# Optimization experiments

Hardware: AMD Instinct MI355X
Metric: run time of the kernel (lower is better)

## Reference

```python
import jax, jax.numpy as jnp
import numpy as np
from jax.scipy.special import logsumexp

N_ITERS = 20


def setup_inputs() -> dict:
    key = jax.random.key(0)
    k1, _ = jax.random.split(key)
    cost_matrix = jax.random.uniform(k1, (64, 1024, 1024), dtype=jnp.float32)
    epsilon = jnp.ones((1,), dtype=jnp.float32)
    return {"cost_matrix": cost_matrix, "epsilon": epsilon}


def reference(cost_matrix, epsilon):
    # log-space Sinkhorn: alternate row / column normalization in log domain
    log_alpha = -cost_matrix / epsilon  # (B, N, N)

    def step(la, _):
        la = la - logsumexp(la, axis=-1, keepdims=True)  # row normalize
        la = la - logsumexp(la, axis=-2, keepdims=True)  # col normalize
        return la, None

    log_alpha, _ = jax.lax.scan(step, log_alpha, None, length=N_ITERS)
    return jnp.exp(log_alpha)
```

## Files before the change

kernel.cpp:

```cpp
#include <hip/hip_runtime.h>
#include <hip/hip_fp16.h>


#define BATCH 64
#define N 1024
#define NITERS 20
#define RPB 64
#define BPB 16
#define NBLK (BATCH * BPB)
#define THREADS 256
#define NU2 (N / 4)
#define NU4 (N / 8)
#define NU4F8 (N / 16)
#define NGRP 64
#define CSUM_ELEMS ((size_t)NITERS * BATCH * N)
#define BAR_WORDS 128

typedef float f32x2 __attribute__((ext_vector_type(2)));

union H2U { __half2 h; unsigned u; };

__device__ __forceinline__ float4 h4_to_f4(uint2 r) {
    H2U a, b;
    a.u = r.x; b.u = r.y;
    float2 fa = __half22float2(a.h);
    float2 fb = __half22float2(b.h);
    return make_float4(fa.x, fa.y, fb.x, fb.y);
}

__device__ __forceinline__ void h8_unpack(uint4 r, float* f) {
    H2U a, b, c, d;
    a.u = r.x; b.u = r.y; c.u = r.z; d.u = r.w;
    float2 fa = __half22float2(a.h), fb = __half22float2(b.h);
    float2 fc = __half22float2(c.h), fd = __half22float2(d.h);
    f[0] = fa.x; f[1] = fa.y; f[2] = fb.x; f[3] = fb.y;
    f[4] = fc.x; f[5] = fc.y; f[6] = fd.x; f[7] = fd.y;
}

__device__ __forceinline__ uint4 h8_pack(const float* f) {
    H2U a, b, c, d;
    a.h = __float22half2_rn(make_float2(f[0], f[1]));
    b.h = __float22half2_rn(make_float2(f[2], f[3]));
    c.h = __float22half2_rn(make_float2(f[4], f[5]));
    d.h = __float22half2_rn(make_float2(f[6], f[7]));
    uint4 r; r.x = a.u; r.y = b.u; r.z = c.u; r.w = d.u;
    return r;
}

__device__ __forceinline__ uint4 pack_fp8_16(const float* k) {
    uint4 r;
    int a;
    a = __builtin_amdgcn_cvt_pk_fp8_f32(k[0],  k[1],  0, false);
    a = __builtin_amdgcn_cvt_pk_fp8_f32(k[2],  k[3],  a, true);
    r.x = (unsigned)a;
    a = __builtin_amdgcn_cvt_pk_fp8_f32(k[4],  k[5],  0, false);
    a = __builtin_amdgcn_cvt_pk_fp8_f32(k[6],  k[7],  a, true);
    r.y = (unsigned)a;
    a = __builtin_amdgcn_cvt_pk_fp8_f32(k[8],  k[9],  0, false);
    a = __builtin_amdgcn_cvt_pk_fp8_f32(k[10], k[11], a, true);
    r.z = (unsigned)a;
    a = __builtin_amdgcn_cvt_pk_fp8_f32(k[12], k[13], 0, false);
    a = __builtin_amdgcn_cvt_pk_fp8_f32(k[14], k[15], a, true);
    r.w = (unsigned)a;
    return r;
}

__device__ __forceinline__ void unpack_fp8_16(uint4 r, float* f) {
    f32x2 p;
    p = __builtin_amdgcn_cvt_pk_f32_fp8((int)r.x, false); f[0]  = p.x; f[1]  = p.y;
    p = __builtin_amdgcn_cvt_pk_f32_fp8((int)r.x, true);  f[2]  = p.x; f[3]  = p.y;
    p = __builtin_amdgcn_cvt_pk_f32_fp8((int)r.y, false); f[4]  = p.x; f[5]  = p.y;
    p = __builtin_amdgcn_cvt_pk_f32_fp8((int)r.y, true);  f[6]  = p.x; f[7]  = p.y;
    p = __builtin_amdgcn_cvt_pk_f32_fp8((int)r.z, false); f[8]  = p.x; f[9]  = p.y;
    p = __builtin_amdgcn_cvt_pk_f32_fp8((int)r.z, true);  f[10] = p.x; f[11] = p.y;
    p = __builtin_amdgcn_cvt_pk_f32_fp8((int)r.w, false); f[12] = p.x; f[13] = p.y;
    p = __builtin_amdgcn_cvt_pk_f32_fp8((int)r.w, true);  f[14] = p.x; f[15] = p.y;
}

__global__ __launch_bounds__(THREADS) void sk_zero(float* __restrict__ csum_all,
                                                   int total) {
    const int i = blockIdx.x * THREADS + threadIdx.x;
    if (i < total) csum_all[i] = 0.0f;
}

__device__ __forceinline__ void gbar(unsigned* __restrict__ bar,
                                     unsigned& gencount) {
    __syncthreads();
    if (threadIdx.x == 0) {
        __threadfence();
        unsigned* grp    = bar;
        unsigned* master = bar + NGRP;
        unsigned* gen    = bar + NGRP + 1;
        const unsigned gid = blockIdx.x & (NGRP - 1);
        if (atomicAdd(&grp[gid], 1u) == (NBLK / NGRP) - 1u) {
            if (atomicAdd(master, 1u) == NGRP - 1u) {
                #pragma unroll
                for (int i = 0; i < NGRP; ++i) atomicExch(&grp[i], 0u);
                atomicExch(master, 0u);
                __threadfence();
                atomicAdd(gen, 1u);
            }
        }
        while (__hip_atomic_load(gen, __ATOMIC_RELAXED,
                                 __HIP_MEMORY_SCOPE_AGENT) == gencount)
            __builtin_amdgcn_s_sleep(2);
        __threadfence();
    }
    __syncthreads();
    ++gencount;
}

__global__ __launch_bounds__(THREADS, 4) void sk_fused(
        const float* __restrict__ C, const float* __restrict__ eps,
        uint4* __restrict__ K16, uint4* __restrict__ K8,
        float* __restrict__ csum, unsigned* __restrict__ bar,
        float* __restrict__ out) {
    __shared__ float4 smc[4][N / 4];
    __shared__ float u_lds[RPB];
    const int t = threadIdx.x;
    const int lane = t & 63, w = t >> 6;
    const int bid = blockIdx.x;
    const int b = bid >> 4, bx = bid & 15;
    const int row0 = bx * RPB + w * 16;
    const int tt = (t + 16 * bx) & 255;
    unsigned gencount = 0;

    {
        const float nie = -1.0f / eps[0];
        const float4* __restrict__ Cp =
            (const float4*)(C + ((size_t)b * N + row0) * N) + lane * 4;
        uint4* __restrict__ Kp16 = K16 + ((size_t)b * N + row0) * NU4 + lane * 2;
        uint4* __restrict__ Kp8  = K8  + ((size_t)b * N + row0) * NU4F8 + lane;

        float colacc[16];
        #pragma unroll
        for (int q = 0; q < 16; ++q) colacc[q] = 0.0f;

        float4 cur[4];
        #pragma unroll
        for (int q = 0; q < 4; ++q) cur[q] = Cp[q];

        #pragma unroll
        for (int i = 0; i < 16; ++i) {
            float4 nxt[4];
            if (i < 15) {
                #pragma unroll
                for (int q = 0; q < 4; ++q) nxt[q] = Cp[(i + 1) * (N / 4) + q];
            }
            float k[16];
            const float* cf = (const float*)cur;
            #pragma unroll
            for (int q = 0; q < 16; ++q) k[q] = __expf(cf[q] * nie);

            Kp16[(size_t)i * NU4]     = h8_pack(k);
            Kp16[(size_t)i * NU4 + 1] = h8_pack(k + 8);
            Kp8[(size_t)i * NU4F8]    = pack_fp8_16(k);

            float s = (((k[0] + k[1]) + (k[2] + k[3])) + ((k[4] + k[5]) + (k[6] + k[7])))
                    + (((k[8] + k[9]) + (k[10] + k[11])) + ((k[12] + k[13]) + (k[14] + k[15])));
            #pragma unroll
            for (int off = 32; off; off >>= 1) s += __shfl_xor(s, off, 64);
            const float ui = 1.0f / s;

            #pragma unroll
            for (int q = 0; q < 16; ++q) colacc[q] += k[q] * ui;

            if (i < 15) {
                #pragma unroll
                for (int q = 0; q < 4; ++q) cur[q] = nxt[q];
            }
        }

        #pragma unroll
        for (int q = 0; q < 4; ++q)
            smc[w][lane * 4 + q] = make_float4(colacc[4 * q], colacc[4 * q + 1],
                                               colacc[4 * q + 2], colacc[4 * q + 3]);
        __syncthreads();
        float4 s0 = smc[0][tt], s1 = smc[1][tt], s2 = smc[2][tt], s3 = smc[3][tt];
        float* cs = csum + b * N + 4 * tt;
        atomicAdd(cs + 0, (s0.x + s1.x) + (s2.x + s3.x));
        atomicAdd(cs + 1, (s0.y + s1.y) + (s2.y + s3.y));
        atomicAdd(cs + 2, (s0.z + s1.z) + (s2.z + s3.z));
        atomicAdd(cs + 3, (s0.w + s1.w) + (s2.w + s3.w));
    }
    gbar(bar, gencount);

    const uint4* __restrict__ Kp8r = K8 + ((size_t)b * N + row0) * NU4F8 + lane;
    #pragma unroll 1
    for (int p = 1; p <= 18; ++p) {
        const float4* __restrict__ cin =
            (const float4*)(csum + (size_t)(p - 1) * BATCH * N + b * N) + lane * 4;
        float vv[16];
        #pragma unroll
        for (int q = 0; q < 4; ++q) {
            float4 c = cin[q];
            vv[4 * q + 0] = 1.0f / c.x;
            vv[4 * q + 1] = 1.0f / c.y;
            vv[4 * q + 2] = 1.0f / c.z;
            vv[4 * q + 3] = 1.0f / c.w;
        }

        float colacc[16];
        #pragma unroll
        for (int q = 0; q < 16; ++q) colacc[q] = 0.0f;

        uint4 buf[4];
        #pragma unroll
        for (int q = 0; q < 4; ++q) buf[q] = Kp8r[(size_t)q * NU4F8];

        __syncthreads();
        #pragma unroll
        for (int i = 0; i < 16; ++i) {
            uint4 nx;
            if (i < 12) nx = Kp8r[(size_t)(i + 4) * NU4F8];

            float k[16];
            unpack_fp8_16(buf[i & 3], k);

            float pa = (k[0] * vv[0] + k[1] * vv[1]) + (k[2] * vv[2] + k[3] * vv[3]);
            float pb = (k[4] * vv[4] + k[5] * vv[5]) + (k[6] * vv[6] + k[7] * vv[7]);
            float pc = (k[8] * vv[8] + k[9] * vv[9]) + (k[10] * vv[10] + k[11] * vv[11]);
            float pd = (k[12] * vv[12] + k[13] * vv[13]) + (k[14] * vv[14] + k[15] * vv[15]);
            float s = (pa + pb) + (pc + pd);

            #pragma unroll
            for (int off = 32; off; off >>= 1) s += __shfl_xor(s, off, 64);
            const float ui = 1.0f / s;

            #pragma unroll
            for (int q = 0; q < 16; ++q) colacc[q] += k[q] * ui;

            if (i < 12) buf[i & 3] = nx;
        }

        #pragma unroll
        for (int q = 0; q < 4; ++q)
            smc[w][lane * 4 + q] = make_float4(colacc[4 * q], colacc[4 * q + 1],
                                               colacc[4 * q + 2], colacc[4 * q + 3]);
        __syncthreads();
        float4 s0 = smc[0][tt], s1 = smc[1][tt], s2 = smc[2][tt], s3 = smc[3][tt];
        float* cs = csum + (size_t)p * BATCH * N + b * N + 4 * tt;
        atomicAdd(cs + 0, (s0.x + s1.x) + (s2.x + s3.x));
        atomicAdd(cs + 1, (s0.y + s1.y) + (s2.y + s3.y));
        atomicAdd(cs + 2, (s0.z + s1.z) + (s2.z + s3.z));
        atomicAdd(cs + 3, (s0.w + s1.w) + (s2.w + s3.w));
        gbar(bar, gencount);
    }

    {
        const float4* __restrict__ cin =
            (const float4*)(csum + (size_t)18 * BATCH * N + b * N) + lane * 4;
        float vv[16];
        #pragma unroll
        for (int q = 0; q < 4; ++q) {
            float4 c = cin[q];
            vv[4 * q + 0] = 1.0f / c.x;
            vv[4 * q + 1] = 1.0f / c.y;
            vv[4 * q + 2] = 1.0f / c.z;
            vv[4 * q + 3] = 1.0f / c.w;
        }

        const uint4* __restrict__ Kp = K16 + ((size_t)b * N + row0) * NU4 + lane * 2;

        float colacc[16];
        #pragma unroll
        for (int q = 0; q < 16; ++q) colacc[q] = 0.0f;

        uint4 c0 = Kp[0], c1 = Kp[1];
        #pragma unroll
        for (int i = 0; i < 16; ++i) {
            uint4 n0, n1;
            if (i < 15) {
                n0 = Kp[(size_t)(i + 1) * NU4];
                n1 = Kp[(size_t)(i + 1) * NU4 + 1];
            }
            float k[16];
            h8_unpack(c0, k);
            h8_unpack(c1, k + 8);

            float pa = (k[0] * vv[0] + k[1] * vv[1]) + (k[2] * vv[2] + k[3] * vv[3]);
            float pb = (k[4] * vv[4] + k[5] * vv[5]) + (k[6] * vv[6] + k[7] * vv[7]);
            float pc = (k[8] * vv[8] + k[9] * vv[9]) + (k[10] * vv[10] + k[11] * vv[11]);
            float pd = (k[12] * vv[12] + k[13] * vv[13]) + (k[14] * vv[14] + k[15] * vv[15]);
            float s = (pa + pb) + (pc + pd);

            #pragma unroll
            for (int off = 32; off; off >>= 1) s += __shfl_xor(s, off, 64);
            const float ui = 1.0f / s;
            if (lane == 0) u_lds[w * 16 + i] = ui;

            #pragma unroll
            for (int q = 0; q < 16; ++q) colacc[q] += k[q] * ui;

            if (i < 15) { c0 = n0; c1 = n1; }
        }

        #pragma unroll
        for (int q = 0; q < 4; ++q)
            smc[w][lane * 4 + q] = make_float4(colacc[4 * q], colacc[4 * q + 1],
                                               colacc[4 * q + 2], colacc[4 * q + 3]);
        __syncthreads();
        float4 s0 = smc[0][tt], s1 = smc[1][tt], s2 = smc[2][tt], s3 = smc[3][tt];
        float* cs = csum + (size_t)19 * BATCH * N + b * N + 4 * tt;
        atomicAdd(cs + 0, (s0.x + s1.x) + (s2.x + s3.x));
        atomicAdd(cs + 1, (s0.y + s1.y) + (s2.y + s3.y));
        atomicAdd(cs + 2, (s0.z + s1.z) + (s2.z + s3.z));
        atomicAdd(cs + 3, (s0.w + s1.w) + (s2.w + s3.w));
    }
    gbar(bar, gencount);

    {
        const float4 ci = ((const float4*)(csum + (size_t)19 * BATCH * N + b * N))[t];
        const float4 vv = make_float4(1.0f / ci.x, 1.0f / ci.y,
                                      1.0f / ci.z, 1.0f / ci.w);
        const size_t rowbase = (size_t)b * N + (size_t)bx * RPB;
        const uint2* __restrict__ K2 = (const uint2*)K16;

        uint2 kc = K2[rowbase * NU2 + t];
        for (int r = 0; r < RPB; ++r) {
            uint2 kn;
            if (r < RPB - 1) kn = K2[(rowbase + r + 1) * NU2 + t];
            const float ur = u_lds[r];
            float4 k = h4_to_f4(kc);
            float4 o;
            o.x = k.x * ur * vv.x;
            o.y = k.y * ur * vv.y;
            o.z = k.z * ur * vv.z;
            o.w = k.w * ur * vv.w;
            ((float4*)(out + (rowbase + r) * N))[t] = o;
            kc = kn;
        }
    }
}


__global__ __launch_bounds__(THREADS) void sk_build(
        const float* __restrict__ C, const float* __restrict__ eps,
        uint4* __restrict__ K16, uint4* __restrict__ K8,
        float* __restrict__ u, float* __restrict__ csum_out) {
    __shared__ float4 smc[4][N / 4];
    const int t = threadIdx.x;
    const int lane = t & 63, w = t >> 6;
    const int b = blockIdx.y;
    const int row0 = blockIdx.x * RPB + w * 16;
    const float nie = -1.0f / eps[0];

    const float4* __restrict__ Cp =
        (const float4*)(C + ((size_t)b * N + row0) * N) + lane * 4;
    uint4* __restrict__ Kp16 = K16 + ((size_t)b * N + row0) * NU4 + lane * 2;
    uint4* __restrict__ Kp8  = K8  + ((size_t)b * N + row0) * NU4F8 + lane;

    float colacc[16];
    #pragma unroll
    for (int q = 0; q < 16; ++q) colacc[q] = 0.0f;

    float4 cur[4];
    #pragma unroll
    for (int q = 0; q < 4; ++q) cur[q] = Cp[q];

    for (int i = 0; i < 16; ++i) {
        float4 nxt[4];
        if (i < 15) {
            #pragma unroll
            for (int q = 0; q < 4; ++q) nxt[q] = Cp[(i + 1) * (N / 4) + q];
        }
        float k[16];
        const float* cf = (const float*)cur;
        #pragma unroll
        for (int q = 0; q < 16; ++q) k[q] = __expf(cf[q] * nie);

        Kp16[(size_t)i * NU4]     = h8_pack(k);
        Kp16[(size_t)i * NU4 + 1] = h8_pack(k + 8);
        Kp8[(size_t)i * NU4F8]    = pack_fp8_16(k);

        float s = (((k[0] + k[1]) + (k[2] + k[3])) + ((k[4] + k[5]) + (k[6] + k[7])))
                + (((k[8] + k[9]) + (k[10] + k[11])) + ((k[12] + k[13]) + (k[14] + k[15])));
        #pragma unroll
        for (int off = 32; off; off >>= 1) s += __shfl_xor(s, off, 64);
        const float ui = 1.0f / s;
        if (lane == 0) u[b * N + row0 + i] = ui;

        #pragma unroll
        for (int q = 0; q < 16; ++q) colacc[q] += k[q] * ui;

        if (i < 15) {
            #pragma unroll
            for (int q = 0; q < 4; ++q) cur[q] = nxt[q];
        }
    }

    #pragma unroll
    for (int q = 0; q < 4; ++q)
        smc[w][lane * 4 + q] = make_float4(colacc[4 * q], colacc[4 * q + 1],
                                           colacc[4 * q + 2], colacc[4 * q + 3]);
    __syncthreads();
    float4 s0 = smc[0][t], s1 = smc[1][t], s2 = smc[2][t], s3 = smc[3][t];
    float* cs = csum_out + b * N + 4 * t;
    atomicAdd(cs + 0, (s0.x + s1.x) + (s2.x + s3.x));
    atomicAdd(cs + 1, (s0.y + s1.y) + (s2.y + s3.y));
    atomicAdd(cs + 2, (s0.z + s1.z) + (s2.z + s3.z));
    atomicAdd(cs + 3, (s0.w + s1.w) + (s2.w + s3.w));
}

__global__ __launch_bounds__(THREADS) void sk_iter8(
        const uint4* __restrict__ K8, const float* __restrict__ csum_in,
        float* __restrict__ csum_out) {
    __shared__ float4 smc[4][N / 4];
    const int t = threadIdx.x;
    const int lane = t & 63, w = t >> 6;
    const int b = blockIdx.y;
    const int row0 = blockIdx.x * RPB + w * 16;

    const float4* __restrict__ cin = (const float4*)(csum_in + b * N) + lane * 4;
    float vv[16];
    #pragma unroll
    for (int q = 0; q < 4; ++q) {
        float4 c = cin[q];
        vv[4 * q + 0] = 1.0f / c.x;
        vv[4 * q + 1] = 1.0f / c.y;
        vv[4 * q + 2] = 1.0f / c.z;
        vv[4 * q + 3] = 1.0f / c.w;
    }

    const uint4* __restrict__ Kp = K8 + ((size_t)b * N + row0) * NU4F8 + lane;

    float colacc[16];
    #pragma unroll
    for (int q = 0; q < 16; ++q) colacc[q] = 0.0f;

    uint4 c0 = Kp[0];
    uint4 c1 = Kp[NU4F8];
    for (int i = 0; i < 16; ++i) {
        uint4 c2;
        if (i < 14) c2 = Kp[(size_t)(i + 2) * NU4F8];

        float k[16];
        unpack_fp8_16(c0, k);

        float pa = (k[0] * vv[0] + k[1] * vv[1]) + (k[2] * vv[2] + k[3] * vv[3]);
        float pb = (k[4] * vv[4] + k[5] * vv[5]) + (k[6] * vv[6] + k[7] * vv[7]);
        float pc = (k[8] * vv[8] + k[9] * vv[9]) + (k[10] * vv[10] + k[11] * vv[11]);
        float pd = (k[12] * vv[12] + k[13] * vv[13]) + (k[14] * vv[14] + k[15] * vv[15]);
        float s = (pa + pb) + (pc + pd);

        #pragma unroll
        for (int off = 32; off; off >>= 1) s += __shfl_xor(s, off, 64);
        const float ui = 1.0f / s;

        #pragma unroll
        for (int q = 0; q < 16; ++q) colacc[q] += k[q] * ui;

        c0 = c1;
        if (i < 14) c1 = c2;
    }

    #pragma unroll
    for (int q = 0; q < 4; ++q)
        smc[w][lane * 4 + q] = make_float4(colacc[4 * q], colacc[4 * q + 1],
                                           colacc[4 * q + 2], colacc[4 * q + 3]);
    __syncthreads();
    float4 s0 = smc[0][t], s1 = smc[1][t], s2 = smc[2][t], s3 = smc[3][t];
    float* cs = csum_out + b * N + 4 * t;
    atomicAdd(cs + 0, (s0.x + s1.x) + (s2.x + s3.x));
    atomicAdd(cs + 1, (s0.y + s1.y) + (s2.y + s3.y));
    atomicAdd(cs + 2, (s0.z + s1.z) + (s2.z + s3.z));
    atomicAdd(cs + 3, (s0.w + s1.w) + (s2.w + s3.w));
}

__global__ __launch_bounds__(THREADS) void sk_iter(
        const uint4* __restrict__ K, const float* __restrict__ csum_in,
        float* __restrict__ u, float* __restrict__ csum_out) {
    __shared__ float4 smc[4][N / 4];
    const int t = threadIdx.x;
    const int lane = t & 63, w = t >> 6;
    const int b = blockIdx.y;
    const int row0 = blockIdx.x * RPB + w * 16;

    const float4* __restrict__ cin = (const float4*)(csum_in + b * N) + lane * 4;
    float vv[16];
    #pragma unroll
    for (int q = 0; q < 4; ++q) {
        float4 c = cin[q];
        vv[4 * q + 0] = 1.0f / c.x;
        vv[4 * q + 1] = 1.0f / c.y;
        vv[4 * q + 2] = 1.0f / c.z;
        vv[4 * q + 3] = 1.0f / c.w;
    }

    const uint4* __restrict__ Kp = K + ((size_t)b * N + row0) * NU4 + lane * 2;

    float colacc[16];
    #pragma unroll
    for (int q = 0; q < 16; ++q) colacc[q] = 0.0f;

    uint4 c0 = Kp[0], c1 = Kp[1];
    for (int i = 0; i < 16; ++i) {
        uint4 n0, n1;
        if (i < 15) {
            n0 = Kp[(size_t)(i + 1) * NU4];
            n1 = Kp[(size_t)(i + 1) * NU4 + 1];
        }
        float k[16];
        h8_unpack(c0, k);
        h8_unpack(c1, k + 8);

        float pa = (k[0] * vv[0] + k[1] * vv[1]) + (k[2] * vv[2] + k[3] * vv[3]);
        float pb = (k[4] * vv[4] + k[5] * vv[5]) + (k[6] * vv[6] + k[7] * vv[7]);
        float pc = (k[8] * vv[8] + k[9] * vv[9]) + (k[10] * vv[10] + k[11] * vv[11]);
        float pd = (k[12] * vv[12] + k[13] * vv[13]) + (k[14] * vv[14] + k[15] * vv[15]);
        float s = (pa + pb) + (pc + pd);

        #pragma unroll
        for (int off = 32; off; off >>= 1) s += __shfl_xor(s, off, 64);
        const float ui = 1.0f / s;
        if (lane == 0) u[b * N + row0 + i] = ui;

        #pragma unroll
        for (int q = 0; q < 16; ++q) colacc[q] += k[q] * ui;

        if (i < 15) { c0 = n0; c1 = n1; }
    }

    #pragma unroll
    for (int q = 0; q < 4; ++q)
        smc[w][lane * 4 + q] = make_float4(colacc[4 * q], colacc[4 * q + 1],
                                           colacc[4 * q + 2], colacc[4 * q + 3]);
    __syncthreads();
    float4 s0 = smc[0][t], s1 = smc[1][t], s2 = smc[2][t], s3 = smc[3][t];
    float* cs = csum_out + b * N + 4 * t;
    atomicAdd(cs + 0, (s0.x + s1.x) + (s2.x + s3.x));
    atomicAdd(cs + 1, (s0.y + s1.y) + (s2.y + s3.y));
    atomicAdd(cs + 2, (s0.z + s1.z) + (s2.z + s3.z));
    atomicAdd(cs + 3, (s0.w + s1.w) + (s2.w + s3.w));
}

__global__ __launch_bounds__(THREADS) void sk_final(
        const uint2* __restrict__ K, const float* __restrict__ u,
        const float* __restrict__ csum_last, float* __restrict__ out) {
    const int t = threadIdx.x;
    const int row = blockIdx.x;
    const int b = blockIdx.y;
    const float ui = u[b * N + row];
    const float4 ci = ((const float4*)(csum_last + b * N))[t];
    const float4 vv = make_float4(1.0f / ci.x, 1.0f / ci.y, 1.0f / ci.z, 1.0f / ci.w);
    const size_t base = (size_t)b * N + row;
    float4 k = h4_to_f4((K + base * NU2)[t]);
    float4 o;
    o.x = k.x * ui * vv.x;
    o.y = k.y * ui * vv.y;
    o.z = k.z * ui * vv.z;
    o.w = k.w * ui * vv.w;
    ((float4*)(out + base * N))[t] = o;
}


__device__ __forceinline__ float block_reduce_broadcast(float val, float* lds) {
    #pragma unroll
    for (int off = 32; off > 0; off >>= 1)
        val += __shfl_xor(val, off, 64);
    const int lane = threadIdx.x & 63;
    const int wid  = threadIdx.x >> 6;
    if (lane == 0) lds[wid] = val;
    __syncthreads();
    float total = lds[0] + lds[1] + lds[2] + lds[3];
    __syncthreads();
    return total;
}

__global__ __launch_bounds__(THREADS) void sink_init(float* __restrict__ v,
                                                     float* __restrict__ colsum) {
    const int i = blockIdx.x * THREADS + threadIdx.x;
    v[i] = 1.0f;
    colsum[i] = 0.0f;
}

__global__ __launch_bounds__(THREADS) void sink_iter(
        const float* __restrict__ C, const float* __restrict__ eps,
        const float* __restrict__ v, float* __restrict__ u,
        float* __restrict__ colsum) {
    __shared__ float lds[4];
    const int t = threadIdx.x;
    const int b = blockIdx.y;
    const int row0 = blockIdx.x * RPB;
    const float neg_inv_eps = -1.0f / eps[0];

    const float4 vv = ((const float4*)(v + b * N))[t];
    const float4* __restrict__ Cp = (const float4*)(C + ((size_t)b * N + row0) * N);

    float4 colacc = make_float4(0.f, 0.f, 0.f, 0.f);
    float4 cur = Cp[t];
    for (int i = 0; i < RPB; ++i) {
        float4 nxt = cur;
        if (i + 1 < RPB)
            nxt = Cp[(size_t)(i + 1) * (N / 4) + t];

        float4 k;
        k.x = __expf(cur.x * neg_inv_eps);
        k.y = __expf(cur.y * neg_inv_eps);
        k.z = __expf(cur.z * neg_inv_eps);
        k.w = __expf(cur.w * neg_inv_eps);

        float s = k.x * vv.x + k.y * vv.y + k.z * vv.z + k.w * vv.w;
        float S = block_reduce_broadcast(s, lds);
        float ui = 1.0f / S;
        if (t == 0) u[b * N + row0 + i] = ui;

        colacc.x += k.x * ui;
        colacc.y += k.y * ui;
        colacc.z += k.z * ui;
        colacc.w += k.w * ui;
        cur = nxt;
    }

    float* cs = colsum + b * N + 4 * t;
    atomicAdd(cs + 0, colacc.x);
    atomicAdd(cs + 1, colacc.y);
    atomicAdd(cs + 2, colacc.z);
    atomicAdd(cs + 3, colacc.w);
}

__global__ __launch_bounds__(THREADS) void sink_fix(float* __restrict__ v,
                                                    float* __restrict__ colsum) {
    const int i = blockIdx.x * THREADS + threadIdx.x;
    v[i] = 1.0f / colsum[i];
    colsum[i] = 0.0f;
}

__global__ __launch_bounds__(THREADS) void sink_final(
        const float* __restrict__ C, const float* __restrict__ eps,
        const float* __restrict__ u, const float* __restrict__ v,
        float* __restrict__ out) {
    const int t = threadIdx.x;
    const int row = blockIdx.x;
    const int b = blockIdx.y;
    const float neg_inv_eps = -1.0f / eps[0];
    const float ui = u[b * N + row];
    const float4 vv = ((const float4*)(v + b * N))[t];
    const size_t base = ((size_t)b * N + row) * N;
    float4 c = ((const float4*)(C + base))[t];
    float4 o;
    o.x = __expf(c.x * neg_inv_eps) * ui * vv.x;
    o.y = __expf(c.y * neg_inv_eps) * ui * vv.y;
    o.z = __expf(c.z * neg_inv_eps) * ui * vv.z;
    o.w = __expf(c.w * neg_inv_eps) * ui * vv.w;
    ((float4*)(out + base))[t] = o;
}


extern "C" void kernel_launch(void* const* d_in, const int* in_sizes, int n_in,
                              void* d_out, int out_size, void* d_ws, size_t ws_size,
                              hipStream_t stream) {
    const float* C   = (const float*)d_in[0];
    const float* eps = (const float*)d_in[1];
    float* out = (float*)d_out;

    const size_t k16_bytes = (size_t)BATCH * N * N * 2;
    const size_t k8_bytes  = (size_t)BATCH * N * N;
    const size_t uv_elems  = (size_t)BATCH * N;
    const size_t needed    = k16_bytes + k8_bytes +
                             (CSUM_ELEMS + BAR_WORDS + uv_elems) * 4;

    if (ws_size >= needed) {
        uint4* K16 = (uint4*)d_ws;
        uint4* K8  = (uint4*)((char*)d_ws + k16_bytes);
        float* csum = (float*)((char*)d_ws + k16_bytes + k8_bytes);
        unsigned* bar = (unsigned*)(csum + CSUM_ELEMS);
        float* u = (float*)(bar + BAR_WORDS);

        static int coop_ok = -1;
        if (coop_ok < 0) {
            int nb = 0;
            hipError_t e = hipOccupancyMaxActiveBlocksPerMultiprocessor(
                &nb, sk_fused, THREADS, 0);
            coop_ok = (e == hipSuccess && nb >= 4) ? 1 : 0;
        }

        const int zero_total = (int)(CSUM_ELEMS + BAR_WORDS);
        sk_zero<<<dim3((zero_total + THREADS - 1) / THREADS), dim3(THREADS),
                  0, stream>>>(csum, zero_total);

        if (coop_ok) {
            sk_fused<<<dim3(NBLK), dim3(THREADS), 0, stream>>>(
                C, eps, K16, K8, csum, bar, out);
        } else {
            sk_build<<<dim3(BPB, BATCH), dim3(THREADS), 0, stream>>>(
                C, eps, K16, K8, u, csum);
            for (int it = 2; it <= NITERS - 1; ++it) {
                sk_iter8<<<dim3(BPB, BATCH), dim3(THREADS), 0, stream>>>(
                    K8, csum + (size_t)(it - 2) * uv_elems,
                    csum + (size_t)(it - 1) * uv_elems);
            }
            sk_iter<<<dim3(BPB, BATCH), dim3(THREADS), 0, stream>>>(
                K16, csum + (size_t)(NITERS - 2) * uv_elems, u,
                csum + (size_t)(NITERS - 1) * uv_elems);
            sk_final<<<dim3(N, BATCH), dim3(THREADS), 0, stream>>>(
                (const uint2*)K16, u, csum + (size_t)(NITERS - 1) * uv_elems, out);
        }
    } else {
        float* u      = (float*)d_ws;
        float* v      = u + uv_elems;
        float* colsum = v + uv_elems;
        sink_init<<<dim3(BATCH * N / THREADS), dim3(THREADS), 0, stream>>>(v, colsum);
        for (int it = 0; it < NITERS; ++it) {
            sink_iter<<<dim3(BPB, BATCH), dim3(THREADS), 0, stream>>>(
                C, eps, v, u, colsum);
            sink_fix<<<dim3(BATCH * N / THREADS), dim3(THREADS), 0, stream>>>(v, colsum);
        }
        sink_final<<<dim3(N, BATCH), dim3(THREADS), 0, stream>>>(C, eps, u, v, out);
    }
}
```

Baseline: 1.002 ms.

## Replace column-sum atomics with double-buffered per-block partials and relaxed barrier

Each block now writes its column partial sums to its own slot in a double-buffered partials array instead of doing float atomicAdds into a per-iteration csum buffer. After each grid barrier, every block reduces the 16 partials for its batch into LDS and computes the reciprocal column scalings there. The grid barrier drops its __threadfence calls in favour of relaxed agent-scope atomics plus an explicit waitcnt, and the large csum zeroing launch is limited to the fallback path. This removes atomic contention and most of the zeroing work, at the cost of 16 times more reads per column reduction and a weaker memory-ordering argument in the barrier.

Result: no change. 1.019 ms (+1.6%).

```diff
diff --git a/kernel.cpp b/kernel.cpp
--- a/kernel.cpp
+++ b/kernel.cpp
@@ -13,8 +13,9 @@
 #define NU4 (N / 8)
 #define NU4F8 (N / 16)
 #define NGRP 64
-#define CSUM_ELEMS ((size_t)NITERS * BATCH * N)
 #define BAR_WORDS 128
+#define PART_ELEMS ((size_t)2 * BATCH * BPB * N)
+#define CSUM_FB_ELEMS ((size_t)NITERS * BATCH * N)
 
 typedef float f32x2 __attribute__((ext_vector_type(2)));
 
@@ -77,34 +78,47 @@
     p = __builtin_amdgcn_cvt_pk_f32_fp8((int)r.w, true);  f[14] = p.x; f[15] = p.y;
 }
 
-__global__ __launch_bounds__(THREADS) void sk_zero(float* __restrict__ csum_all,
+__device__ __forceinline__ float cload(const float* p) {
+    return __hip_atomic_load((float*)p, __ATOMIC_RELAXED, __HIP_MEMORY_SCOPE_AGENT);
+}
+__device__ __forceinline__ void cstore(float* p, float v) {
+    __hip_atomic_store(p, v, __ATOMIC_RELAXED, __HIP_MEMORY_SCOPE_AGENT);
+}
+
+__global__ __launch_bounds__(THREADS) void sk_zero(float* __restrict__ buf,
                                                    int total) {
     const int i = blockIdx.x * THREADS + threadIdx.x;
-    if (i < total) csum_all[i] = 0.0f;
+    if (i < total) buf[i] = 0.0f;
 }
 
 __device__ __forceinline__ void gbar(unsigned* __restrict__ bar,
                                      unsigned& gencount) {
     __syncthreads();
     if (threadIdx.x == 0) {
-        __threadfence();
+        asm volatile("" ::: "memory");
         unsigned* grp    = bar;
         unsigned* master = bar + NGRP;
         unsigned* gen    = bar + NGRP + 1;
         const unsigned gid = blockIdx.x & (NGRP - 1);
-        if (atomicAdd(&grp[gid], 1u) == (NBLK / NGRP) - 1u) {
-            if (atomicAdd(master, 1u) == NGRP - 1u) {
+        if (__hip_atomic_fetch_add(&grp[gid], 1u, __ATOMIC_RELAXED,
+                                   __HIP_MEMORY_SCOPE_AGENT) == (NBLK / NGRP) - 1u) {
+            if (__hip_atomic_fetch_add(master, 1u, __ATOMIC_RELAXED,
+                                       __HIP_MEMORY_SCOPE_AGENT) == NGRP - 1u) {
                 #pragma unroll
-                for (int i = 0; i < NGRP; ++i) atomicExch(&grp[i], 0u);
-                atomicExch(master, 0u);
-                __threadfence();
-                atomicAdd(gen, 1u);
+                for (int i = 0; i < NGRP; ++i)
+                    __hip_atomic_store(&grp[i], 0u, __ATOMIC_RELAXED,
+                                       __HIP_MEMORY_SCOPE_AGENT);
+                __hip_atomic_store(master, 0u, __ATOMIC_RELAXED,
+                                   __HIP_MEMORY_SCOPE_AGENT);
+                asm volatile("s_waitcnt vmcnt(0)" ::: "memory");
+                __hip_atomic_fetch_add(gen, 1u, __ATOMIC_RELAXED,
+                                       __HIP_MEMORY_SCOPE_AGENT);
             }
         }
         while (__hip_atomic_load(gen, __ATOMIC_RELAXED,
                                  __HIP_MEMORY_SCOPE_AGENT) == gencount)
             __builtin_amdgcn_s_sleep(2);
-        __threadfence();
+        asm volatile("" ::: "memory");
     }
     __syncthreads();
     ++gencount;
@@ -113,16 +127,16 @@
 __global__ __launch_bounds__(THREADS, 4) void sk_fused(
         const float* __restrict__ C, const float* __restrict__ eps,
         uint4* __restrict__ K16, uint4* __restrict__ K8,
-        float* __restrict__ csum, unsigned* __restrict__ bar,
+        float* __restrict__ part, unsigned* __restrict__ bar,
         float* __restrict__ out) {
     __shared__ float4 smc[4][N / 4];
+    __shared__ float vsh[N];
     __shared__ float u_lds[RPB];
     const int t = threadIdx.x;
     const int lane = t & 63, w = t >> 6;
     const int bid = blockIdx.x;
     const int b = bid >> 4, bx = bid & 15;
     const int row0 = bx * RPB + w * 16;
-    const int tt = (t + 16 * bx) & 255;
     unsigned gencount = 0;
 
     {
@@ -176,29 +190,39 @@
             smc[w][lane * 4 + q] = make_float4(colacc[4 * q], colacc[4 * q + 1],
                                                colacc[4 * q + 2], colacc[4 * q + 3]);
         __syncthreads();
-        float4 s0 = smc[0][tt], s1 = smc[1][tt], s2 = smc[2][tt], s3 = smc[3][tt];
-        float* cs = csum + b * N + 4 * tt;
-        atomicAdd(cs + 0, (s0.x + s1.x) + (s2.x + s3.x));
-        atomicAdd(cs + 1, (s0.y + s1.y) + (s2.y + s3.y));
-        atomicAdd(cs + 2, (s0.z + s1.z) + (s2.z + s3.z));
-        atomicAdd(cs + 3, (s0.w + s1.w) + (s2.w + s3.w));
+        float4 s0 = smc[0][t], s1 = smc[1][t], s2 = smc[2][t], s3 = smc[3][t];
+        float* pw = part + (((size_t)0 * BATCH + b) * BPB + bx) * N + 4 * t;
+        cstore(pw + 0, (s0.x + s1.x) + (s2.x + s3.x));
+        cstore(pw + 1, (s0.y + s1.y) + (s2.y + s3.y));
+        cstore(pw + 2, (s0.z + s1.z) + (s2.z + s3.z));
+        cstore(pw + 3, (s0.w + s1.w) + (s2.w + s3.w));
     }
     gbar(bar, gencount);
 
     const uint4* __restrict__ Kp8r = K8 + ((size_t)b * N + row0) * NU4F8 + lane;
     #pragma unroll 1
     for (int p = 1; p <= 18; ++p) {
-        const float4* __restrict__ cin =
-            (const float4*)(csum + (size_t)(p - 1) * BATCH * N + b * N) + lane * 4;
+        {
+            const float* pb =
+                part + (((size_t)((p - 1) & 1) * BATCH + b) * BPB) * N + 4 * t;
+            float a0 = 0.f, a1 = 0.f, a2 = 0.f, a3 = 0.f;
+            #pragma unroll
+            for (int j = 0; j < BPB; ++j) {
+                const float* pj = pb + (size_t)j * N;
+                a0 += cload(pj + 0);
+                a1 += cload(pj + 1);
+                a2 += cload(pj + 2);
+                a3 += cload(pj + 3);
+            }
+            vsh[4 * t + 0] = 1.0f / a0;
+            vsh[4 * t + 1] = 1.0f / a1;
+            vsh[4 * t + 2] = 1.0f / a2;
+            vsh[4 * t + 3] = 1.0f / a3;
+        }
+        __syncthreads();
         float vv[16];
         #pragma unroll
-        for (int q = 0; q < 4; ++q) {
-            float4 c = cin[q];
-            vv[4 * q + 0] = 1.0f / c.x;
-            vv[4 * q + 1] = 1.0f / c.y;
-            vv[4 * q + 2] = 1.0f / c.z;
-            vv[4 * q + 3] = 1.0f / c.w;
-        }
+        for (int e = 0; e < 16; ++e) vv[e] = vsh[lane * 16 + e];
 
         float colacc[16];
         #pragma unroll
@@ -208,7 +232,6 @@
         #pragma unroll
         for (int q = 0; q < 4; ++q) buf[q] = Kp8r[(size_t)q * NU4F8];
 
-        __syncthreads();
         #pragma unroll
         for (int i = 0; i < 16; ++i) {
             uint4 nx;
@@ -238,27 +261,36 @@
             smc[w][lane * 4 + q] = make_float4(colacc[4 * q], colacc[4 * q + 1],
                                                colacc[4 * q + 2], colacc[4 * q + 3]);
         __syncthreads();
-        float4 s0 = smc[0][tt], s1 = smc[1][tt], s2 = smc[2][tt], s3 = smc[3][tt];
-        float* cs = csum + (size_t)p * BATCH * N + b * N + 4 * tt;
-        atomicAdd(cs + 0, (s0.x + s1.x) + (s2.x + s3.x));
-        atomicAdd(cs + 1, (s0.y + s1.y) + (s2.y + s3.y));
-        atomicAdd(cs + 2, (s0.z + s1.z) + (s2.z + s3.z));
-        atomicAdd(cs + 3, (s0.w + s1.w) + (s2.w + s3.w));
+        float4 s0 = smc[0][t], s1 = smc[1][t], s2 = smc[2][t], s3 = smc[3][t];
+        float* pw = part + (((size_t)(p & 1) * BATCH + b) * BPB + bx) * N + 4 * t;
+        cstore(pw + 0, (s0.x + s1.x) + (s2.x + s3.x));
+        cstore(pw + 1, (s0.y + s1.y) + (s2.y + s3.y));
+        cstore(pw + 2, (s0.z + s1.z) + (s2.z + s3.z));
+        cstore(pw + 3, (s0.w + s1.w) + (s2.w + s3.w));
         gbar(bar, gencount);
     }
 
     {
-        const float4* __restrict__ cin =
-            (const float4*)(csum + (size_t)18 * BATCH * N + b * N) + lane * 4;
+        {
+            const float* pb = part + (((size_t)0 * BATCH + b) * BPB) * N + 4 * t;
+            float a0 = 0.f, a1 = 0.f, a2 = 0.f, a3 = 0.f;
+            #pragma unroll
+            for (int j = 0; j < BPB; ++j) {
+                const float* pj = pb + (size_t)j * N;
+                a0 += cload(pj + 0);
+                a1 += cload(pj + 1);
+                a2 += cload(pj + 2);
+                a3 += cload(pj + 3);
+            }
+            vsh[4 * t + 0] = 1.0f / a0;
+            vsh[4 * t + 1] = 1.0f / a1;
+            vsh[4 * t + 2] = 1.0f / a2;
+            vsh[4 * t + 3] = 1.0f / a3;
+        }
+        __syncthreads();
         float vv[16];
         #pragma unroll
-        for (int q = 0; q < 4; ++q) {
-            float4 c = cin[q];
-            vv[4 * q + 0] = 1.0f / c.x;
-            vv[4 * q + 1] = 1.0f / c.y;
-            vv[4 * q + 2] = 1.0f / c.z;
-            vv[4 * q + 3] = 1.0f / c.w;
-        }
+        for (int e = 0; e < 16; ++e) vv[e] = vsh[lane * 16 + e];
 
         const uint4* __restrict__ Kp = K16 + ((size_t)b * N + row0) * NU4 + lane * 2;
 
@@ -300,19 +332,35 @@
             smc[w][lane * 4 + q] = make_float4(colacc[4 * q], colacc[4 * q + 1],
                                                colacc[4 * q + 2], colacc[4 * q + 3]);
         __syncthreads();
-        float4 s0 = smc[0][tt], s1 = smc[1][tt], s2 = smc[2][tt], s3 = smc[3][tt];
-        float* cs = csum + (size_t)19 * BATCH * N + b * N + 4 * tt;
-        atomicAdd(cs + 0, (s0.x + s1.x) + (s2.x + s3.x));
-        atomicAdd(cs + 1, (s0.y + s1.y) + (s2.y + s3.y));
-        atomicAdd(cs + 2, (s0.z + s1.z) + (s2.z + s3.z));
-        atomicAdd(cs + 3, (s0.w + s1.w) + (s2.w + s3.w));
+        float4 s0 = smc[0][t], s1 = smc[1][t], s2 = smc[2][t], s3 = smc[3][t];
+        float* pw = part + (((size_t)1 * BATCH + b) * BPB + bx) * N + 4 * t;
+        cstore(pw + 0, (s0.x + s1.x) + (s2.x + s3.x));
+        cstore(pw + 1, (s0.y + s1.y) + (s2.y + s3.y));
+        cstore(pw + 2, (s0.z + s1.z) + (s2.z + s3.z));
+        cstore(pw + 3, (s0.w + s1.w) + (s2.w + s3.w));
     }
     gbar(bar, gencount);
 
     {
-        const float4 ci = ((const float4*)(csum + (size_t)19 * BATCH * N + b * N))[t];
-        const float4 vv = make_float4(1.0f / ci.x, 1.0f / ci.y,
-                                      1.0f / ci.z, 1.0f / ci.w);
+        {
+            const float* pb = part + (((size_t)1 * BATCH + b) * BPB) * N + 4 * t;
+            float a0 = 0.f, a1 = 0.f, a2 = 0.f, a3 = 0.f;
+            #pragma unroll
+            for (int j = 0; j < BPB; ++j) {
+                const float* pj = pb + (size_t)j * N;
+                a0 += cload(pj + 0);
+                a1 += cload(pj + 1);
+                a2 += cload(pj + 2);
+                a3 += cload(pj + 3);
+            }
+            vsh[4 * t + 0] = 1.0f / a0;
+            vsh[4 * t + 1] = 1.0f / a1;
+            vsh[4 * t + 2] = 1.0f / a2;
+            vsh[4 * t + 3] = 1.0f / a3;
+        }
+        __syncthreads();
+        const float4 vvf = make_float4(vsh[4 * t + 0], vsh[4 * t + 1],
+                                       vsh[4 * t + 2], vsh[4 * t + 3]);
         const size_t rowbase = (size_t)b * N + (size_t)bx * RPB;
         const uint2* __restrict__ K2 = (const uint2*)K16;
 
@@ -323,10 +371,10 @@
             const float ur = u_lds[r];
             float4 k = h4_to_f4(kc);
             float4 o;
-            o.x = k.x * ur * vv.x;
-            o.y = k.y * ur * vv.y;
-            o.z = k.z * ur * vv.z;
-            o.w = k.w * ur * vv.w;
+            o.x = k.x * ur * vvf.x;
+            o.y = k.y * ur * vvf.y;
+            o.z = k.z * ur * vvf.z;
+            o.w = k.w * ur * vvf.w;
             ((float4*)(out + (rowbase + r) * N))[t] = o;
             kc = kn;
         }
@@ -654,18 +702,20 @@
     const float* eps = (const float*)d_in[1];
     float* out = (float*)d_out;
 
-    const size_t k16_bytes = (size_t)BATCH * N * N * 2;
-    const size_t k8_bytes  = (size_t)BATCH * N * N;
-    const size_t uv_elems  = (size_t)BATCH * N;
-    const size_t needed    = k16_bytes + k8_bytes +
-                             (CSUM_ELEMS + BAR_WORDS + uv_elems) * 4;
+    const size_t k16_bytes  = (size_t)BATCH * N * N * 2;
+    const size_t k8_bytes   = (size_t)BATCH * N * N;
+    const size_t part_bytes = PART_ELEMS * 4;
+    const size_t uv_elems   = (size_t)BATCH * N;
+    const size_t needed     = k16_bytes + k8_bytes + part_bytes +
+                              BAR_WORDS * 4 + uv_elems * 4 + CSUM_FB_ELEMS * 4;
 
     if (ws_size >= needed) {
-        uint4* K16 = (uint4*)d_ws;
-        uint4* K8  = (uint4*)((char*)d_ws + k16_bytes);
-        float* csum = (float*)((char*)d_ws + k16_bytes + k8_bytes);
-        unsigned* bar = (unsigned*)(csum + CSUM_ELEMS);
-        float* u = (float*)(bar + BAR_WORDS);
+        uint4* K16    = (uint4*)d_ws;
+        uint4* K8     = (uint4*)((char*)d_ws + k16_bytes);
+        float* part   = (float*)((char*)d_ws + k16_bytes + k8_bytes);
+        unsigned* bar = (unsigned*)(part + PART_ELEMS);
+        float* u      = (float*)(bar + BAR_WORDS);
+        float* csum   = u + uv_elems;
 
         static int coop_ok = -1;
         if (coop_ok < 0) {
@@ -675,14 +725,14 @@
             coop_ok = (e == hipSuccess && nb >= 4) ? 1 : 0;
         }
 
-        const int zero_total = (int)(CSUM_ELEMS + BAR_WORDS);
-        sk_zero<<<dim3((zero_total + THREADS - 1) / THREADS), dim3(THREADS),
-                  0, stream>>>(csum, zero_total);
-
         if (coop_ok) {
+            sk_zero<<<dim3(1), dim3(THREADS), 0, stream>>>((float*)bar, BAR_WORDS);
             sk_fused<<<dim3(NBLK), dim3(THREADS), 0, stream>>>(
-                C, eps, K16, K8, csum, bar, out);
+                C, eps, K16, K8, part, bar, out);
         } else {
+            const int zero_total = (int)CSUM_FB_ELEMS;
+            sk_zero<<<dim3((zero_total + THREADS - 1) / THREADS), dim3(THREADS),
+                      0, stream>>>(csum, zero_total);
             sk_build<<<dim3(BPB, BATCH), dim3(THREADS), 0, stream>>>(
                 C, eps, K16, K8, u, csum);
             for (int it = 2; it <= NITERS - 1; ++it) {
```
